# Performance work log

Measured on AMD Instinct MI355X. Metric: run time of the kernel, lower is better.

The kernel has to match this reference:

```python
import jax, jax.numpy as jnp
import numpy as np

EPS = 1e-12
W_MAX = 0.8
ALPHA_MAX = 1.5
T = 10
ETA = 0.2
ALPHA_SCALE = 1.0
N = 50000
IN_DIM = 512
HID = 256
C = 8
EH = 64
E2 = 400000  # undirected pairs; E = 2*E2 directed edges


def setup_inputs() -> dict:
    key = jax.random.key(0)
    ks = jax.random.split(key, 12)
    x = jax.random.normal(ks[0], (N, IN_DIM), jnp.float32)
    src0 = jax.random.randint(ks[1], (E2,), 0, N)
    dst0 = jax.random.randint(ks[2], (E2,), 0, N)
    edge_index = jnp.concatenate([jnp.stack([src0, dst0]), jnp.stack([dst0, src0])], axis=1)
    rev = jnp.concatenate([jnp.arange(E2) + E2, jnp.arange(E2)])
    def lin(k, i, o):
        return jax.random.normal(k, (i, o), jnp.float32) * (2.0 / i) ** 0.5
    enc_w1 = lin(ks[3], IN_DIM, HID); enc_b1 = jnp.zeros((HID,), jnp.float32)
    enc_w2 = lin(ks[4], HID, C); enc_b2 = jnp.zeros((C,), jnp.float32)
    edge_w1 = lin(ks[5], 2 * HID + 2, EH); edge_b1 = jnp.zeros((EH,), jnp.float32)
    edge_w2 = lin(ks[6], EH, 1); edge_b2 = jnp.zeros((1,), jnp.float32)
    bound = (6.0 / (C + C)) ** 0.5  # xavier_uniform
    R_raw = jax.random.uniform(ks[7], (C, C), jnp.float32, -bound, bound) + 0.5 * jnp.eye(C, dtype=jnp.float32)
    R_scale_log = jnp.float32(0.0)
    msg_logit = jnp.float32(-3.0)
    return dict(x=x, edge_index=edge_index, rev=rev,
                enc_w1=enc_w1, enc_b1=enc_b1, enc_w2=enc_w2, enc_b2=enc_b2,
                edge_w1=edge_w1, edge_b1=edge_b1, edge_w2=edge_w2, edge_b2=edge_b2,
                R_raw=R_raw, R_scale_log=R_scale_log, msg_logit=msg_logit)


def reference(x, edge_index, rev, enc_w1, enc_b1, enc_w2, enc_b2,
              edge_w1, edge_b1, edge_w2, edge_b2, R_raw, R_scale_log, msg_logit):
    num_nodes = x.shape[0]
    src, dst = edge_index[0], edge_index[1]
    # unary encoder (mlp type, eval mode -> no dropout)
    h = jax.nn.relu(x @ enc_w1 + enc_b1)
    logits = h @ enc_w2 + enc_b2
    log_phi = jax.nn.log_softmax(logits, axis=-1)  # [N, C]
    # structural edge features from out-degree of src
    deg = jax.ops.segment_sum(jnp.ones_like(src, jnp.float32), src, num_segments=num_nodes)
    logdeg = jnp.log(deg + 1.0)
    a, b = logdeg[src], logdeg[dst]
    struct = jnp.stack([a + b, jnp.abs(a - b)], axis=-1)  # [E, 2]
    # learned symmetric edge weights -> per-edge kernel K
    hs, hd = h[src], h[dst]
    edge_in = jnp.concatenate([hs * hd, jnp.abs(hs - hd), struct], axis=-1)  # [E, 2H+2]
    eh = jax.nn.relu(edge_in @ edge_w1 + edge_b1)
    w_raw = (eh @ edge_w2 + edge_b2)[:, 0]
    w = W_MAX * jax.nn.sigmoid(w_raw)
    w = 0.5 * (w + w[rev])
    R = 0.5 * (R_raw + R_raw.T)
    R = (jax.nn.softplus(R_scale_log) + 1e-06) * jnp.tanh(R)
    K = jnp.exp(w[:, None, None] * R[None])  # [E, C, C]
    degc = jnp.maximum(deg, 1.0)
    edge_norm = (degc[src] * degc[dst]) ** -0.5  # [E]
    alpha = ALPHA_MAX * jax.nn.sigmoid(msg_logit) * ALPHA_SCALE
    lp_src = log_phi[src]
    m = jax.nn.softmax(lp_src, axis=-1)  # init_unary=True

    def step(m, _):
        f = jnp.einsum('ec,ecd->ed', m, K)
        log_f = jnp.log(jnp.maximum(f, EPS)) * edge_norm[:, None]
        sum_in = jax.ops.segment_sum(log_f, dst, num_segments=num_nodes)
        excl = sum_in[src] - log_f[rev]
        m_new = jax.nn.softmax(lp_src + alpha * excl, axis=-1)
        m = (1.0 - ETA) * m + ETA * m_new
        m = jnp.maximum(m, EPS)
        m = m / m.sum(axis=-1, keepdims=True)
        return m, None

    m, _ = jax.lax.scan(step, m, None, length=T)
    # beliefs
    f = jnp.einsum('ec,ecd->ed', m, K)
    log_f = jnp.log(jnp.maximum(f, EPS)) * edge_norm[:, None]
    sum_in = jax.ops.segment_sum(log_f, dst, num_segments=num_nodes)
    beliefs = jax.nn.softmax(log_phi + alpha * sum_in, axis=-1)
    return beliefs
```

## Files before the change

### kernel.cpp

```cpp
#include <hip/hip_runtime.h>
#include <cstddef>
#include <cstdint>

typedef _Float16 h4 __attribute__((ext_vector_type(4)));
typedef _Float16 h8 __attribute__((ext_vector_type(8)));
typedef float    f4 __attribute__((ext_vector_type(4)));
typedef int      i4 __attribute__((ext_vector_type(4)));

#define NN      50000
#define IND     512
#define HIDN    256
#define E2P     400000
#define EDD     800000
#define NBLK    196
#define EBLK    1563

#define OFF_HF16    ((size_t)0)
#define OFF_LOGF    ((size_t)0)
#define OFF_Z       ((size_t)25600000)
#define OFF_DEG     ((size_t)28800000)
#define OFF_LOGDEG  ((size_t)29000000)
#define OFF_DEGC    ((size_t)29200000)
#define OFF_BASE    ((size_t)29400000)
#define OFF_CNT     ((size_t)29600000)
#define OFF_BLK     ((size_t)29800000)
#define OFF_WT      ((size_t)29804096)
#define OFF_BT      ((size_t)30066240)
#define OFF_RS      ((size_t)30135872)
#define OFF_WSYM    ((size_t)30136384)
#define OFF_POS     ((size_t)31736384)
#define OFF_ORDER   ((size_t)34936384)
#define OFF_BASE2   ((size_t)36536384)
#define OFF_OFS2    ((size_t)36736384)
#define OFF_PRC     ((size_t)36936384)
#define OFF_WN      ((size_t)43336384)
#define OFF_M       ((size_t)46536384)
#define OFF_EIS     ((size_t)59336384)
#define WS_NEED     ((size_t)62536384)

__global__ void k_deg(const int* __restrict__ ei, int* __restrict__ deg,
                      int* __restrict__ cnt2) {
    int e = blockIdx.x * 256 + threadIdx.x;
    int v = ei[e];
    atomicAdd(&deg[v], 1);
    if (e < E2P) atomicAdd(&cnt2[v], 1);
}

__global__ void k_node(const int* __restrict__ deg, float* __restrict__ logdeg,
                       float* __restrict__ degc) {
    int n = blockIdx.x * 256 + threadIdx.x;
    if (n < NN) {
        float d = (float)deg[n];
        logdeg[n] = logf(d + 1.0f);
        degc[n]   = fmaxf(d, 1.0f);
    }
}

__global__ void k_scan1(const int* __restrict__ deg, int* __restrict__ incl,
                        int* __restrict__ blk) {
    __shared__ int sm[256];
    int i = blockIdx.x * 256 + threadIdx.x;
    int v = (i < NN) ? deg[i] : 0;
    sm[threadIdx.x] = v;
    __syncthreads();
    for (int off = 1; off < 256; off <<= 1) {
        int t = (threadIdx.x >= off) ? sm[threadIdx.x - off] : 0;
        __syncthreads();
        sm[threadIdx.x] += t;
        __syncthreads();
    }
    if (i < NN) incl[i] = sm[threadIdx.x];
    if (threadIdx.x == 255) blk[blockIdx.x] = sm[255];
}

__global__ void k_scan2(int* __restrict__ blk) {
    __shared__ int sm[256];
    int v = (threadIdx.x < NBLK) ? blk[threadIdx.x] : 0;
    sm[threadIdx.x] = v;
    __syncthreads();
    for (int off = 1; off < 256; off <<= 1) {
        int t = (threadIdx.x >= off) ? sm[threadIdx.x - off] : 0;
        __syncthreads();
        sm[threadIdx.x] += t;
        __syncthreads();
    }
    if (threadIdx.x < NBLK) blk[threadIdx.x] = sm[threadIdx.x];
}

__global__ void k_scan3(const int* __restrict__ incl, const int* __restrict__ deg,
                        const int* __restrict__ blk, int* __restrict__ base) {
    int i = blockIdx.x * 256 + threadIdx.x;
    if (i < NN) {
        int off = (blockIdx.x > 0) ? blk[blockIdx.x - 1] : 0;
        base[i] = off + incl[i] - deg[i];
    }
}

__global__ void k_pos(const int* __restrict__ ei, const int* __restrict__ base,
                      int* __restrict__ cnt, int* __restrict__ pos) {
    int e = blockIdx.x * 256 + threadIdx.x;
    int dstn = ei[EDD + e];
    pos[e] = base[dstn] + atomicAdd(&cnt[dstn], 1);
}

__global__ void k_order(const int* __restrict__ ei, const int* __restrict__ base2,
                        int* __restrict__ ofs2, int* __restrict__ order) {
    int p = blockIdx.x * 256 + threadIdx.x;
    if (p < E2P) {
        int s = ei[p];
        order[base2[s] + atomicAdd(&ofs2[s], 1)] = p;
    }
}

__global__ void k_gath(const int* __restrict__ ei, const int* __restrict__ order,
                       int2* __restrict__ eiS) {
    int i = blockIdx.x * 256 + threadIdx.x;
    if (i < E2P) {
        int p = order[i];
        eiS[i] = make_int2(ei[p], ei[EDD + p]);
    }
}

__global__ void k_prep(const float* __restrict__ enc_w1, const float* __restrict__ edge_w1,
                       const float* __restrict__ R_raw, const float* __restrict__ Rsl,
                       const float* __restrict__ mlog,
                       _Float16* __restrict__ Wt, _Float16* __restrict__ Bt,
                       float* __restrict__ Rs) {
    int gid = blockIdx.x * 256 + threadIdx.x;
    if (gid < 256 * 512) {
        int n = gid >> 9, k = gid & 511;
        Wt[n * 512 + k] = (_Float16)enc_w1[k * 256 + n];
        return;
    }
    int g2 = gid - 256 * 512;
    if (g2 < 64 * 544) {
        int n = g2 / 544, k = g2 - n * 544;
        float v = 0.0f;
        if (k < 512) {
            int tm = k >> 5, r = k & 31;
            int qq = r >> 3, jj = (r >> 1) & 3, typ = k & 1;
            int c = (tm >> 1) * 32 + qq * 8 + (tm & 1) * 4 + jj;
            v = edge_w1[(typ ? 256 + c : c) * 64 + n];
        } else if (k < 514) {
            v = edge_w1[k * 64 + n];
        }
        Bt[n * 544 + k] = (_Float16)v;
        return;
    }
    int g3 = g2 - 64 * 544;
    if (g3 < 64) {
        int c = g3 >> 3, d = g3 & 7;
        float rv = 0.5f * (R_raw[c * 8 + d] + R_raw[d * 8 + c]);
        float s  = log1pf(expf(Rsl[0])) + 1e-6f;
        Rs[g3] = s * tanhf(rv);
        return;
    }
    if (g3 == 64) {
        Rs[64] = 1.5f / (1.0f + expf(-mlog[0]));
    }
}

__global__ __launch_bounds__(256) void k_enc(const float* __restrict__ x,
                                             const _Float16* __restrict__ Wt,
                                             const float* __restrict__ b1,
                                             _Float16* __restrict__ hf) {
    __shared__ _Float16 XL[64 * 40];
    __shared__ _Float16 WL[256 * 40];
    const int tid = threadIdx.x;
    const int wid = tid >> 6;
    const int lane = tid & 63;
    const int l15 = lane & 15;
    const int q = lane >> 4;
    const int m0 = blockIdx.x * 64;

    f4 acc[16];
#pragma unroll
    for (int i = 0; i < 16; i++) acc[i] = (f4){0.f, 0.f, 0.f, 0.f};

    const int xr = tid >> 2;
    const int xs = tid & 3;
    const int gr = m0 + xr;

    for (int kt = 0; kt < 16; kt++) {
        __syncthreads();
        f4 xv0 = (f4){0, 0, 0, 0}, xv1 = (f4){0, 0, 0, 0};
        if (gr < NN) {
            const f4* xp = (const f4*)(x + (size_t)gr * IND + kt * 32 + xs * 8);
            xv0 = xp[0]; xv1 = xp[1];
        }
        h8 xh;
#pragma unroll
        for (int u = 0; u < 4; u++) { xh[u] = (_Float16)xv0[u]; xh[4 + u] = (_Float16)xv1[u]; }
        *(h8*)&XL[xr * 40 + xs * 8] = xh;
#pragma unroll
        for (int rep = 0; rep < 4; rep++) {
            int cid = rep * 256 + tid;
            int n = cid >> 2;
            int off = (cid & 3) * 8;
            h8 wv = *(const h8*)(Wt + (size_t)n * IND + kt * 32 + off);
            *(h8*)&WL[n * 40 + off] = wv;
        }
        __syncthreads();
        h8 a = *(const h8*)&XL[(wid * 16 + l15) * 40 + q * 8];
#pragma unroll
        for (int nt = 0; nt < 16; nt++) {
            h8 b = *(const h8*)&WL[(nt * 16 + l15) * 40 + q * 8];
            acc[nt] = __builtin_amdgcn_mfma_f32_16x16x32_f16(a, b, acc[nt], 0, 0, 0);
        }
    }
#pragma unroll
    for (int nt = 0; nt < 16; nt++) {
        int col = nt * 16 + l15;
        float bv = b1[col];
#pragma unroll
        for (int reg = 0; reg < 4; reg++) {
            int row = m0 + wid * 16 + q * 4 + reg;
            if (row < NN) {
                float v = acc[nt][reg] + bv;
                hf[(size_t)row * HIDN + col] = (_Float16)fmaxf(v, 0.f);
            }
        }
    }
}

__global__ void k_logits(const _Float16* __restrict__ hf, const float* __restrict__ w2,
                         const float* __restrict__ b2, float* __restrict__ Z) {
    __shared__ float w2L[2048];
    for (int i = threadIdx.x; i < 2048; i += 256) w2L[i] = w2[i];
    __syncthreads();
    int n = blockIdx.x * 256 + threadIdx.x;
    if (n >= NN) return;
    float sum[8];
#pragma unroll
    for (int c = 0; c < 8; c++) sum[c] = b2[c];
    for (int kb = 0; kb < 32; kb++) {
        h8 hv = *(const h8*)(hf + (size_t)n * HIDN + kb * 8);
#pragma unroll
        for (int u = 0; u < 8; u++) {
            float hx = (float)hv[u];
            const float* wr = &w2L[(kb * 8 + u) * 8];
#pragma unroll
            for (int c = 0; c < 8; c++) sum[c] += hx * wr[c];
        }
    }
    float mx = sum[0];
#pragma unroll
    for (int c = 1; c < 8; c++) mx = fmaxf(mx, sum[c]);
    float se = 0.f;
#pragma unroll
    for (int c = 0; c < 8; c++) se += __expf(sum[c] - mx);
    float lse = __logf(se);
#pragma unroll
    for (int c = 0; c < 8; c++) Z[(size_t)n * 16 + c] = sum[c] - mx - lse;
}

__global__ __launch_bounds__(256) void k_edge(const int2* __restrict__ eiS,
        const _Float16* __restrict__ hf, const float* __restrict__ logdeg,
        const _Float16* __restrict__ BtG, const float* __restrict__ eb1,
        const float* __restrict__ ew2, const float* __restrict__ eb2,
        float* __restrict__ wsym2) {
    __shared__ _Float16 BtL[64 * 136];
    const int tid = threadIdx.x;
    const int wid = tid >> 6;
    const int lane = tid & 63;
    const int l15 = lane & 15;
    const int q = lane >> 4;
    const int eb = blockIdx.x * 128;

    int sidx[2], didx[2];
    float la[2], lb[2];
#pragma unroll
    for (int mt = 0; mt < 2; mt++) {
        int e = eb + wid * 32 + mt * 16 + l15;
        int2 sd = eiS[e];
        sidx[mt] = sd.x;
        didx[mt] = sd.y;
        la[mt] = logdeg[sidx[mt]];
        lb[mt] = logdeg[didx[mt]];
    }

    f4 acc[2][4];
#pragma unroll
    for (int a = 0; a < 2; a++)
#pragma unroll
        for (int b = 0; b < 4; b++) acc[a][b] = (f4){0.f, 0.f, 0.f, 0.f};

    const _Float16* hq = hf + q * 8;
    h8 curS[2], curD[2];
#pragma unroll
    for (int mt = 0; mt < 2; mt++) {
        curS[mt] = *(const h8*)(hq + (size_t)sidx[mt] * HIDN);
        curD[mt] = *(const h8*)(hq + (size_t)didx[mt] * HIDN);
    }

    for (int ph = 0; ph < 4; ph++) {
        __syncthreads();
        {
            const int r = tid & 63;
            const int cb = tid >> 6;
            const int kbase = ph * 128;
#pragma unroll
            for (int i = 0; i < 4; i++) {
                int ck = cb + i * 4;
                *(h8*)&BtL[r * 136 + ck * 8] =
                    *(const h8*)(BtG + (size_t)r * 544 + kbase + ck * 8);
            }
        }
        __syncthreads();
#pragma unroll
        for (int kk2 = 0; kk2 < 2; kk2++) {
            const int kk = ph * 2 + kk2;
            h8 nxtS[2], nxtD[2];
            if (kk < 7) {
                const int c1 = (kk + 1) * 32;
#pragma unroll
                for (int mt = 0; mt < 2; mt++) {
                    nxtS[mt] = *(const h8*)(hq + (size_t)sidx[mt] * HIDN + c1);
                    nxtD[mt] = *(const h8*)(hq + (size_t)didx[mt] * HIDN + c1);
                }
            }
            const int ko = kk2 * 64 + q * 8;
            {
                h8 a0[2];
#pragma unroll
                for (int mt = 0; mt < 2; mt++) {
#pragma unroll
                    for (int j = 0; j < 4; j++) {
                        float x1 = (float)curS[mt][j], x2 = (float)curD[mt][j];
                        a0[mt][2 * j]     = (_Float16)(x1 * x2);
                        a0[mt][2 * j + 1] = (_Float16)fabsf(x1 - x2);
                    }
                }
                h8 bf[4];
#pragma unroll
                for (int nt = 0; nt < 4; nt++)
                    bf[nt] = *(const h8*)&BtL[(nt * 16 + l15) * 136 + ko];
#pragma unroll
                for (int mt = 0; mt < 2; mt++)
#pragma unroll
                    for (int nt = 0; nt < 4; nt++)
                        acc[mt][nt] = __builtin_amdgcn_mfma_f32_16x16x32_f16(a0[mt], bf[nt], acc[mt][nt], 0, 0, 0);
            }
            {
                h8 a1[2];
#pragma unroll
                for (int mt = 0; mt < 2; mt++) {
#pragma unroll
                    for (int j = 0; j < 4; j++) {
                        float x1 = (float)curS[mt][4 + j], x2 = (float)curD[mt][4 + j];
                        a1[mt][2 * j]     = (_Float16)(x1 * x2);
                        a1[mt][2 * j + 1] = (_Float16)fabsf(x1 - x2);
                    }
                }
                h8 bf[4];
#pragma unroll
                for (int nt = 0; nt < 4; nt++)
                    bf[nt] = *(const h8*)&BtL[(nt * 16 + l15) * 136 + ko + 32];
#pragma unroll
                for (int mt = 0; mt < 2; mt++)
#pragma unroll
                    for (int nt = 0; nt < 4; nt++)
                        acc[mt][nt] = __builtin_amdgcn_mfma_f32_16x16x32_f16(a1[mt], bf[nt], acc[mt][nt], 0, 0, 0);
            }
            if (kk < 7) {
#pragma unroll
                for (int mt = 0; mt < 2; mt++) { curS[mt] = nxtS[mt]; curD[mt] = nxtD[mt]; }
            }
        }
    }

    __syncthreads();
    {
        const int r = tid & 63, ck = tid >> 6;
        *(h8*)&BtL[r * 136 + ck * 8] = *(const h8*)(BtG + (size_t)r * 544 + 512 + ck * 8);
    }
    __syncthreads();
    {
        h8 bf[4];
#pragma unroll
        for (int nt = 0; nt < 4; nt++)
            bf[nt] = *(const h8*)&BtL[(nt * 16 + l15) * 136 + q * 8];
#pragma unroll
        for (int mt = 0; mt < 2; mt++) {
            h8 a = (h8){0, 0, 0, 0, 0, 0, 0, 0};
            if (q == 0) {
                a[0] = (_Float16)(la[mt] + lb[mt]);
                a[1] = (_Float16)fabsf(la[mt] - lb[mt]);
            }
#pragma unroll
            for (int nt = 0; nt < 4; nt++)
                acc[mt][nt] = __builtin_amdgcn_mfma_f32_16x16x32_f16(a, bf[nt], acc[mt][nt], 0, 0, 0);
        }
    }

    float b1v[4], w2v[4];
#pragma unroll
    for (int nt = 0; nt < 4; nt++) {
        int col = nt * 16 + l15;
        b1v[nt] = eb1[col];
        w2v[nt] = ew2[col];
    }
    const float b2s = eb2[0];
    float part[2][4];
#pragma unroll
    for (int mt = 0; mt < 2; mt++)
#pragma unroll
        for (int reg = 0; reg < 4; reg++) {
            float s = 0.f;
#pragma unroll
            for (int nt = 0; nt < 4; nt++) {
                float v = acc[mt][nt][reg] + b1v[nt];
                s += fmaxf(v, 0.f) * w2v[nt];
            }
            part[mt][reg] = s;
        }
#pragma unroll
    for (int off = 1; off < 16; off <<= 1)
#pragma unroll
        for (int mt = 0; mt < 2; mt++)
#pragma unroll
            for (int reg = 0; reg < 4; reg++)
                part[mt][reg] += __shfl_xor(part[mt][reg], off, 64);
    if (l15 == 0) {
#pragma unroll
        for (int mt = 0; mt < 2; mt++)
#pragma unroll
            for (int reg = 0; reg < 4; reg++) {
                int er = eb + wid * 32 + mt * 16 + q * 4 + reg;
                if (er < E2P) {
                    float xr = part[mt][reg] + b2s;
                    wsym2[er] = 0.8f / (1.0f + __expf(-xr));
                }
            }
    }
}


__device__ __forceinline__ void kprod(const float* __restrict__ RsL, float w,
                                      const float* me, const float* mr,
                                      float* fe, float* fr) {
#pragma unroll
    for (int d = 0; d < 8; d++) { fe[d] = 0.f; fr[d] = 0.f; }
#pragma unroll
    for (int c = 0; c < 8; c++) {
        {
            float kv = __expf(w * RsL[c * 8 + c]);
            fe[c] += me[c] * kv;
            fr[c] += mr[c] * kv;
        }
#pragma unroll
        for (int d = c + 1; d < 8; d++) {
            float kv = __expf(w * RsL[c * 8 + d]);
            fe[d] += me[c] * kv; fr[d] += mr[c] * kv;
            fe[c] += me[d] * kv; fr[c] += mr[d] * kv;
        }
    }
}

__global__ __launch_bounds__(256) void k_init(const int2* __restrict__ eiS,
        const float* __restrict__ wsym2, const float* __restrict__ degc,
        const float* __restrict__ Rs, const float* __restrict__ Z,
        const int* __restrict__ pos, const int* __restrict__ order,
        i4* __restrict__ prc, float2* __restrict__ wn,
        _Float16* __restrict__ M, _Float16* __restrict__ logf) {
    __shared__ float RsL[64];
    const int tid = threadIdx.x;
    if (tid < 64) RsL[tid] = Rs[tid];
    __syncthreads();
    int i = blockIdx.x * 256 + tid;
    if (i >= E2P) return;
    int p = order[i];
    int2 sd = eiS[i];
    int sp = sd.x, dp = sd.y;
    float w = wsym2[i];
    float nrm = rsqrtf(degc[sp] * degc[dp]);
    int pz0 = pos[p], pz1 = pos[E2P + p];
    prc[i] = (i4){sp, dp, pz0, pz1};
    wn[i] = make_float2(w, nrm);
    const f4* Zs = (const f4*)(Z + (size_t)sp * 16);
    const f4* Zd = (const f4*)(Z + (size_t)dp * 16);
    f4 ls0 = Zs[0], ls1 = Zs[1], ld0 = Zd[0], ld1 = Zd[1];
    float lps[8], lpd[8];
#pragma unroll
    for (int u = 0; u < 4; u++) { lps[u] = ls0[u]; lps[4+u] = ls1[u]; lpd[u] = ld0[u]; lpd[4+u] = ld1[u]; }
    float me[8], mr[8];
    {
        float mx = lps[0], mx2 = lpd[0];
#pragma unroll
        for (int d = 1; d < 8; d++) { mx = fmaxf(mx, lps[d]); mx2 = fmaxf(mx2, lpd[d]); }
        float s = 0.f, s2 = 0.f;
#pragma unroll
        for (int d = 0; d < 8; d++) { me[d] = __expf(lps[d] - mx); s += me[d];
                                      mr[d] = __expf(lpd[d] - mx2); s2 += mr[d]; }
        float rs = 1.f / s, rs2 = 1.f / s2;
#pragma unroll
        for (int d = 0; d < 8; d++) { me[d] *= rs; mr[d] *= rs2; }
    }
    {
        h8 mh, mh2;
#pragma unroll
        for (int d = 0; d < 8; d++) { mh[d] = (_Float16)me[d]; mh2[d] = (_Float16)mr[d]; }
        *(h8*)(M + (size_t)i * 16)     = mh;
        *(h8*)(M + (size_t)i * 16 + 8) = mh2;
    }
    float fe[8], fr[8];
    kprod(RsL, w, me, mr, fe, fr);
    h8 le, lr;
#pragma unroll
    for (int d = 0; d < 8; d++) {
        le[d] = (_Float16)(__logf(fmaxf(fe[d], 1e-12f)) * nrm);
        lr[d] = (_Float16)(__logf(fmaxf(fr[d], 1e-12f)) * nrm);
    }
    *(h8*)(logf + (size_t)pz0 * 8) = le;
    *(h8*)(logf + (size_t)pz1 * 8) = lr;
}

__global__ __launch_bounds__(256) void k_bpF(const i4* __restrict__ prc,
        const float2* __restrict__ wn, const float* __restrict__ Rs,
        const float* __restrict__ Z, _Float16* __restrict__ M,
        _Float16* __restrict__ logf) {
    __shared__ float RsL[64];
    const int tid = threadIdx.x;
    if (tid < 64) RsL[tid] = Rs[tid];
    __syncthreads();
    int i = blockIdx.x * 256 + tid;
    if (i >= E2P) return;
    i4 c4 = prc[i];
    const int sp = c4[0], dp = c4[1], pz0 = c4[2], pz1 = c4[3];
    float2 wnv = wn[i];
    const float w = wnv.x, nrm = wnv.y;
    const float alpha = Rs[64];
    h8 lfh0 = *(const h8*)(logf + (size_t)pz0 * 8);
    h8 lfh1 = *(const h8*)(logf + (size_t)pz1 * 8);
    h8 mhe = *(const h8*)(M + (size_t)i * 16);
    h8 mhr = *(const h8*)(M + (size_t)i * 16 + 8);
    float me[8], mr[8], lfe[8], lfr[8];
#pragma unroll
    for (int d = 0; d < 8; d++) {
        me[d] = (float)mhe[d];  mr[d] = (float)mhr[d];
        lfe[d] = (float)lfh0[d]; lfr[d] = (float)lfh1[d];
    }
    const f4* Zs = (const f4*)(Z + (size_t)sp * 16);
    const f4* Zd = (const f4*)(Z + (size_t)dp * 16);
    f4 ls0 = Zs[0], ls1 = Zs[1], ss0 = Zs[2], ss1 = Zs[3];
    f4 ld0 = Zd[0], ld1 = Zd[1], sd0 = Zd[2], sd1 = Zd[3];
    float te[8], tr[8];
#pragma unroll
    for (int u = 0; u < 4; u++) {
        te[u]     = ls0[u] + alpha * (ss0[u] - lfr[u]);
        te[4 + u] = ls1[u] + alpha * (ss1[u] - lfr[4 + u]);
        tr[u]     = ld0[u] + alpha * (sd0[u] - lfe[u]);
        tr[4 + u] = ld1[u] + alpha * (sd1[u] - lfe[4 + u]);
    }
    float m1[8], m2[8];
    {
        float mx = te[0], mx2 = tr[0];
#pragma unroll
        for (int d = 1; d < 8; d++) { mx = fmaxf(mx, te[d]); mx2 = fmaxf(mx2, tr[d]); }
        float s = 0.f, s2 = 0.f;
#pragma unroll
        for (int d = 0; d < 8; d++) { m1[d] = __expf(te[d] - mx); s += m1[d];
                                      m2[d] = __expf(tr[d] - mx2); s2 += m2[d]; }
        float rs = 1.f / s, rs2 = 1.f / s2;
        float t1 = 0.f, t2 = 0.f;
#pragma unroll
        for (int d = 0; d < 8; d++) {
            m1[d] = fmaxf(0.8f * me[d] + 0.2f * m1[d] * rs, 1e-12f);  t1 += m1[d];
            m2[d] = fmaxf(0.8f * mr[d] + 0.2f * m2[d] * rs2, 1e-12f); t2 += m2[d];
        }
        float rt1 = 1.f / t1, rt2 = 1.f / t2;
#pragma unroll
        for (int d = 0; d < 8; d++) { m1[d] *= rt1; m2[d] *= rt2; }
    }
    {
        h8 mh, mh2;
#pragma unroll
        for (int d = 0; d < 8; d++) { mh[d] = (_Float16)m1[d]; mh2[d] = (_Float16)m2[d]; }
        *(h8*)(M + (size_t)i * 16)     = mh;
        *(h8*)(M + (size_t)i * 16 + 8) = mh2;
    }
    float fe2[8], fr2[8];
    kprod(RsL, w, m1, m2, fe2, fr2);
    h8 le, lr;
#pragma unroll
    for (int d = 0; d < 8; d++) {
        le[d] = (_Float16)(__logf(fmaxf(fe2[d], 1e-12f)) * nrm);
        lr[d] = (_Float16)(__logf(fmaxf(fr2[d], 1e-12f)) * nrm);
    }
    *(h8*)(logf + (size_t)pz0 * 8) = le;
    *(h8*)(logf + (size_t)pz1 * 8) = lr;
}

__global__ void k_sum(const _Float16* __restrict__ logf, const int* __restrict__ base,
                      const int* __restrict__ deg, float* __restrict__ Z,
                      const float* __restrict__ Rs, float* __restrict__ out, int fin) {
    int g = blockIdx.x * 256 + threadIdx.x;
    int n = g >> 3;
    if (n >= NN) return;
    int j = threadIdx.x & 7;
    int b = base[n], cnt = deg[n];
    float acc[8];
#pragma unroll
    for (int d = 0; d < 8; d++) acc[d] = 0.f;
    for (int s = j; s < cnt; s += 8) {
        h8 v = *(const h8*)(logf + (size_t)(b + s) * 8);
#pragma unroll
        for (int d = 0; d < 8; d++) acc[d] += (float)v[d];
    }
    int lane = threadIdx.x & 63;
    float v4[4], v2[2], r;
    {
        bool hi = (lane & 4) != 0;
#pragma unroll
        for (int i = 0; i < 4; i++) {
            float send = hi ? acc[i] : acc[i + 4];
            float recv = __shfl_xor(send, 4, 64);
            v4[i] = (hi ? acc[i + 4] : acc[i]) + recv;
        }
    }
    {
        bool hi = (lane & 2) != 0;
#pragma unroll
        for (int i = 0; i < 2; i++) {
            float send = hi ? v4[i] : v4[i + 2];
            float recv = __shfl_xor(send, 2, 64);
            v2[i] = (hi ? v4[i + 2] : v4[i]) + recv;
        }
    }
    {
        bool hi = (lane & 1) != 0;
        float send = hi ? v2[0] : v2[1];
        float recv = __shfl_xor(send, 1, 64);
        r = (hi ? v2[1] : v2[0]) + recv;
    }
    if (!fin) {
        Z[(size_t)n * 16 + 8 + j] = r;
    } else {
        float alpha = Rs[64];
        float v = Z[(size_t)n * 16 + j] + alpha * r;
        float mx = v;
        mx = fmaxf(mx, __shfl_xor(mx, 1, 64));
        mx = fmaxf(mx, __shfl_xor(mx, 2, 64));
        mx = fmaxf(mx, __shfl_xor(mx, 4, 64));
        float ex = __expf(v - mx);
        float s = ex;
        s += __shfl_xor(s, 1, 64); s += __shfl_xor(s, 2, 64); s += __shfl_xor(s, 4, 64);
        out[(size_t)n * 8 + j] = ex / s;
    }
}

extern "C" void kernel_launch(void* const* d_in, const int* in_sizes, int n_in,
                              void* d_out, int out_size, void* d_ws, size_t ws_size,
                              hipStream_t stream) {
    if (ws_size < WS_NEED) return;
    const float* x        = (const float*)d_in[0];
    const int*   ei       = (const int*)d_in[1];
    const float* enc_w1   = (const float*)d_in[3];
    const float* enc_b1   = (const float*)d_in[4];
    const float* enc_w2   = (const float*)d_in[5];
    const float* enc_b2   = (const float*)d_in[6];
    const float* edge_w1  = (const float*)d_in[7];
    const float* edge_b1  = (const float*)d_in[8];
    const float* edge_w2  = (const float*)d_in[9];
    const float* edge_b2  = (const float*)d_in[10];
    const float* R_raw    = (const float*)d_in[11];
    const float* Rsl      = (const float*)d_in[12];
    const float* mlog     = (const float*)d_in[13];

    char* ws = (char*)d_ws;
    _Float16* hf     = (_Float16*)(ws + OFF_HF16);
    _Float16* logfb  = (_Float16*)(ws + OFF_LOGF);
    float* Zb        = (float*)(ws + OFF_Z);
    int*   deg       = (int*)  (ws + OFF_DEG);
    float* logdeg    = (float*)(ws + OFF_LOGDEG);
    float* degc      = (float*)(ws + OFF_DEGC);
    int*   baseA     = (int*)  (ws + OFF_BASE);
    int*   cnt       = (int*)  (ws + OFF_CNT);
    int*   blk       = (int*)  (ws + OFF_BLK);
    _Float16* Wt     = (_Float16*)(ws + OFF_WT);
    _Float16* Bt     = (_Float16*)(ws + OFF_BT);
    float* Rs        = (float*)(ws + OFF_RS);
    float* wsym2     = (float*)(ws + OFF_WSYM);
    int*   pos       = (int*)  (ws + OFF_POS);
    int*   order     = (int*)  (ws + OFF_ORDER);
    int*   base2     = (int*)  (ws + OFF_BASE2);
    int*   ofs2      = (int*)  (ws + OFF_OFS2);
    i4*    prc       = (i4*)   (ws + OFF_PRC);
    float2* wnb      = (float2*)(ws + OFF_WN);
    _Float16* Mb     = (_Float16*)(ws + OFF_M);
    int2*  eiS       = (int2*) (ws + OFF_EIS);
    float* outp      = (float*)d_out;

    hipMemsetAsync(deg, 0, (size_t)NN * 4, stream);
    hipMemsetAsync(ofs2, 0, (size_t)NN * 4, stream);
    k_deg<<<dim3(EDD / 256), dim3(256), 0, stream>>>(ei, deg, ofs2);
    k_node<<<dim3(NBLK), dim3(256), 0, stream>>>(deg, logdeg, degc);
    k_prep<<<dim3((256 * 512 + 64 * 544 + 65 + 255) / 256), dim3(256), 0, stream>>>(
        enc_w1, edge_w1, R_raw, Rsl, mlog, Wt, Bt, Rs);
    k_scan1<<<dim3(NBLK), dim3(256), 0, stream>>>(deg, cnt , blk);
    k_scan2<<<dim3(1), dim3(256), 0, stream>>>(blk);
    k_scan3<<<dim3(NBLK), dim3(256), 0, stream>>>(cnt, deg, blk, baseA);
    hipMemsetAsync(cnt, 0, (size_t)NN * 4, stream);
    k_pos<<<dim3(EDD / 256), dim3(256), 0, stream>>>(ei, baseA, cnt, pos);
    k_scan1<<<dim3(NBLK), dim3(256), 0, stream>>>(ofs2, cnt, blk);
    k_scan2<<<dim3(1), dim3(256), 0, stream>>>(blk);
    k_scan3<<<dim3(NBLK), dim3(256), 0, stream>>>(cnt, ofs2, blk, base2);
    hipMemsetAsync(ofs2, 0, (size_t)NN * 4, stream);
    k_order<<<dim3(EBLK), dim3(256), 0, stream>>>(ei, base2, ofs2, order);
    k_gath<<<dim3(EBLK), dim3(256), 0, stream>>>(ei, order, eiS);
    k_enc<<<dim3((NN + 63) / 64), dim3(256), 0, stream>>>(x, Wt, enc_b1, hf);
    k_logits<<<dim3(NBLK), dim3(256), 0, stream>>>(hf, enc_w2, enc_b2, Zb);
    k_edge<<<dim3(E2P / 128), dim3(256), 0, stream>>>(eiS, hf, logdeg, Bt, edge_b1,
                                                      edge_w2, edge_b2, wsym2);
    k_init<<<dim3(EBLK), dim3(256), 0, stream>>>(eiS, wsym2, degc, Rs, Zb, pos, order,
                                                 prc, wnb, Mb, logfb);
    k_sum<<<dim3((NN * 8 + 255) / 256), dim3(256), 0, stream>>>(logfb, baseA, deg, Zb,
                                                                Rs, outp, 0);
    for (int t = 0; t < 10; t++) {
        k_bpF<<<dim3(EBLK), dim3(256), 0, stream>>>(prc, wnb, Rs, Zb, Mb, logfb);
        k_sum<<<dim3((NN * 8 + 255) / 256), dim3(256), 0, stream>>>(logfb, baseA, deg, Zb,
                                                                    Rs, outp, (t == 9) ? 1 : 0);
    }
    (void)in_sizes; (void)n_in; (void)out_size;
}
```

Before: 820.0 us.

## Sort edges by 2D src/dst bucket, recompute log_f in-step, retile encoder, swizzle XCD blocks

```diff
diff --git a/kernel.cpp b/kernel.cpp
--- a/kernel.cpp
+++ b/kernel.cpp
@@ -13,37 +13,51 @@
 #define E2P     400000
 #define EDD     800000
 #define NBLK    196
+#define SCN     50176
 #define EBLK    1563
 
 #define OFF_HF16    ((size_t)0)
 #define OFF_LOGF    ((size_t)0)
 #define OFF_Z       ((size_t)25600000)
 #define OFF_DEG     ((size_t)28800000)
-#define OFF_LOGDEG  ((size_t)29000000)
-#define OFF_DEGC    ((size_t)29200000)
-#define OFF_BASE    ((size_t)29400000)
-#define OFF_CNT     ((size_t)29600000)
-#define OFF_BLK     ((size_t)29800000)
-#define OFF_WT      ((size_t)29804096)
-#define OFF_BT      ((size_t)30066240)
-#define OFF_RS      ((size_t)30135872)
-#define OFF_WSYM    ((size_t)30136384)
-#define OFF_POS     ((size_t)31736384)
-#define OFF_ORDER   ((size_t)34936384)
-#define OFF_BASE2   ((size_t)36536384)
-#define OFF_OFS2    ((size_t)36736384)
-#define OFF_PRC     ((size_t)36936384)
-#define OFF_WN      ((size_t)43336384)
-#define OFF_M       ((size_t)46536384)
-#define OFF_EIS     ((size_t)59336384)
-#define WS_NEED     ((size_t)62536384)
+#define OFF_LOGDEG  ((size_t)29004800)
+#define OFF_DEGC    ((size_t)29204800)
+#define OFF_BASE    ((size_t)29404800)
+#define OFF_CNT     ((size_t)29609600)
+#define OFF_BLK     ((size_t)29814400)
+#define OFF_WT      ((size_t)29818496)
+#define OFF_BT      ((size_t)30080640)
+#define OFF_RS      ((size_t)30150272)
+#define OFF_WSYM    ((size_t)30150784)
+#define OFF_POS     ((size_t)31750784)
+#define OFF_ORDER   ((size_t)34950784)
+#define OFF_BASE2   ((size_t)36550784)
+#define OFF_OFS2    ((size_t)36755584)
+#define OFF_PRC     ((size_t)36960384)
+#define OFF_WN      ((size_t)43360384)
+#define OFF_M       ((size_t)46560384)
+#define OFF_EIS     ((size_t)59360384)
+#define WS_NEED     ((size_t)62560384)
+
+__device__ __forceinline__ int key2(int s, int d) {
+    return ((s >> 10) << 10) | (d >> 6);
+}
+
+__device__ __forceinline__ int xcd_swz(int bid, int nwg) {
+    int q = nwg >> 3, r = nwg & 7;
+    int x = bid & 7, idx = bid >> 3;
+    return (x < r ? x * (q + 1) : r * (q + 1) + (x - r) * q) + idx;
+}
 
 __global__ void k_deg(const int* __restrict__ ei, int* __restrict__ deg,
                       int* __restrict__ cnt2) {
     int e = blockIdx.x * 256 + threadIdx.x;
     int v = ei[e];
     atomicAdd(&deg[v], 1);
-    if (e < E2P) atomicAdd(&cnt2[v], 1);
+    if (e < E2P) {
+        int d = ei[EDD + e];
+        atomicAdd(&cnt2[key2(v, d)], 1);
+    }
 }
 
 __global__ void k_node(const int* __restrict__ deg, float* __restrict__ logdeg,
@@ -60,7 +74,7 @@
                         int* __restrict__ blk) {
     __shared__ int sm[256];
     int i = blockIdx.x * 256 + threadIdx.x;
-    int v = (i < NN) ? deg[i] : 0;
+    int v = deg[i];
     sm[threadIdx.x] = v;
     __syncthreads();
     for (int off = 1; off < 256; off <<= 1) {
@@ -69,7 +83,7 @@
         sm[threadIdx.x] += t;
         __syncthreads();
     }
-    if (i < NN) incl[i] = sm[threadIdx.x];
+    incl[i] = sm[threadIdx.x];
     if (threadIdx.x == 255) blk[blockIdx.x] = sm[255];
 }
 
@@ -90,10 +104,8 @@
 __global__ void k_scan3(const int* __restrict__ incl, const int* __restrict__ deg,
                         const int* __restrict__ blk, int* __restrict__ base) {
     int i = blockIdx.x * 256 + threadIdx.x;
-    if (i < NN) {
-        int off = (blockIdx.x > 0) ? blk[blockIdx.x - 1] : 0;
-        base[i] = off + incl[i] - deg[i];
-    }
+    int off = (blockIdx.x > 0) ? blk[blockIdx.x - 1] : 0;
+    base[i] = off + incl[i] - deg[i];
 }
 
 __global__ void k_pos(const int* __restrict__ ei, const int* __restrict__ base,
@@ -107,8 +119,8 @@
                         int* __restrict__ ofs2, int* __restrict__ order) {
     int p = blockIdx.x * 256 + threadIdx.x;
     if (p < E2P) {
-        int s = ei[p];
-        order[base2[s] + atomicAdd(&ofs2[s], 1)] = p;
+        int k = key2(ei[p], ei[EDD + p]);
+        order[base2[k] + atomicAdd(&ofs2[k], 1)] = p;
     }
 }
 
@@ -164,59 +176,84 @@
                                              const _Float16* __restrict__ Wt,
                                              const float* __restrict__ b1,
                                              _Float16* __restrict__ hf) {
-    __shared__ _Float16 XL[64 * 40];
-    __shared__ _Float16 WL[256 * 40];
+    __shared__ _Float16 XL[32 * 32];
+    __shared__ _Float16 WL[256 * 32];
     const int tid = threadIdx.x;
     const int wid = tid >> 6;
     const int lane = tid & 63;
     const int l15 = lane & 15;
     const int q = lane >> 4;
-    const int m0 = blockIdx.x * 64;
-
-    f4 acc[16];
-#pragma unroll
-    for (int i = 0; i < 16; i++) acc[i] = (f4){0.f, 0.f, 0.f, 0.f};
+    const int m0 = blockIdx.x * 32;
+    const int mt = wid & 1;
+    const int nh = wid >> 1;
+
+    f4 acc[8];
+#pragma unroll
+    for (int i = 0; i < 8; i++) acc[i] = (f4){0.f, 0.f, 0.f, 0.f};
 
     const int xr = tid >> 2;
     const int xs = tid & 3;
+    const bool xact = (tid < 128);
     const int gr = m0 + xr;
+
+    h8 xreg = (h8){0, 0, 0, 0, 0, 0, 0, 0};
+    if (xact && gr < NN) {
+        const f4* xp = (const f4*)(x + (size_t)gr * IND + xs * 8);
+        f4 a0 = xp[0], a1 = xp[1];
+#pragma unroll
+        for (int u = 0; u < 4; u++) { xreg[u] = (_Float16)a0[u]; xreg[4 + u] = (_Float16)a1[u]; }
+    }
+    h8 wreg[4];
+#pragma unroll
+    for (int rep = 0; rep < 4; rep++) {
+        int id = rep * 256 + tid;
+        int n = id >> 2, c = id & 3;
+        wreg[rep] = *(const h8*)(Wt + (size_t)n * IND + c * 8);
+    }
 
     for (int kt = 0; kt < 16; kt++) {
         __syncthreads();
-        f4 xv0 = (f4){0, 0, 0, 0}, xv1 = (f4){0, 0, 0, 0};
-        if (gr < NN) {
-            const f4* xp = (const f4*)(x + (size_t)gr * IND + kt * 32 + xs * 8);
-            xv0 = xp[0]; xv1 = xp[1];
-        }
-        h8 xh;
-#pragma unroll
-        for (int u = 0; u < 4; u++) { xh[u] = (_Float16)xv0[u]; xh[4 + u] = (_Float16)xv1[u]; }
-        *(h8*)&XL[xr * 40 + xs * 8] = xh;
+        if (xact) *(h8*)&XL[xr * 32 + ((xs + (xr >> 1)) & 3) * 8] = xreg;
 #pragma unroll
         for (int rep = 0; rep < 4; rep++) {
-            int cid = rep * 256 + tid;
-            int n = cid >> 2;
-            int off = (cid & 3) * 8;
-            h8 wv = *(const h8*)(Wt + (size_t)n * IND + kt * 32 + off);
-            *(h8*)&WL[n * 40 + off] = wv;
+            int id = rep * 256 + tid;
+            int n = id >> 2, c = id & 3;
+            *(h8*)&WL[n * 32 + ((c + (n >> 1)) & 3) * 8] = wreg[rep];
         }
         __syncthreads();
-        h8 a = *(const h8*)&XL[(wid * 16 + l15) * 40 + q * 8];
-#pragma unroll
-        for (int nt = 0; nt < 16; nt++) {
-            h8 b = *(const h8*)&WL[(nt * 16 + l15) * 40 + q * 8];
-            acc[nt] = __builtin_amdgcn_mfma_f32_16x16x32_f16(a, b, acc[nt], 0, 0, 0);
-        }
-    }
-#pragma unroll
-    for (int nt = 0; nt < 16; nt++) {
-        int col = nt * 16 + l15;
+        if (kt < 15) {
+            const int kc = (kt + 1) * 32;
+            if (xact && gr < NN) {
+                const f4* xp = (const f4*)(x + (size_t)gr * IND + kc + xs * 8);
+                f4 a0 = xp[0], a1 = xp[1];
+#pragma unroll
+                for (int u = 0; u < 4; u++) { xreg[u] = (_Float16)a0[u]; xreg[4 + u] = (_Float16)a1[u]; }
+            }
+#pragma unroll
+            for (int rep = 0; rep < 4; rep++) {
+                int id = rep * 256 + tid;
+                int n = id >> 2, c = id & 3;
+                wreg[rep] = *(const h8*)(Wt + (size_t)n * IND + kc + c * 8);
+            }
+        }
+        const int ar = mt * 16 + l15;
+        h8 a = *(const h8*)&XL[ar * 32 + ((q + (ar >> 1)) & 3) * 8];
+#pragma unroll
+        for (int nt8 = 0; nt8 < 8; nt8++) {
+            int r2 = (nh * 8 + nt8) * 16 + l15;
+            h8 b = *(const h8*)&WL[r2 * 32 + ((q + (r2 >> 1)) & 3) * 8];
+            acc[nt8] = __builtin_amdgcn_mfma_f32_16x16x32_f16(a, b, acc[nt8], 0, 0, 0);
+        }
+    }
+#pragma unroll
+    for (int nt8 = 0; nt8 < 8; nt8++) {
+        int col = (nh * 8 + nt8) * 16 + l15;
         float bv = b1[col];
 #pragma unroll
         for (int reg = 0; reg < 4; reg++) {
-            int row = m0 + wid * 16 + q * 4 + reg;
+            int row = m0 + mt * 16 + q * 4 + reg;
             if (row < NN) {
-                float v = acc[nt][reg] + bv;
+                float v = acc[nt8][reg] + bv;
                 hf[(size_t)row * HIDN + col] = (_Float16)fmaxf(v, 0.f);
             }
         }
@@ -265,7 +302,7 @@
     const int lane = tid & 63;
     const int l15 = lane & 15;
     const int q = lane >> 4;
-    const int eb = blockIdx.x * 128;
+    const int eb = xcd_swz(blockIdx.x, gridDim.x) * 128;
 
     int sidx[2], didx[2];
     float la[2], lb[2];
@@ -296,12 +333,12 @@
     for (int ph = 0; ph < 4; ph++) {
         __syncthreads();
         {
-            const int r = tid & 63;
-            const int cb = tid >> 6;
+            const int r = tid >> 2;
+            const int c0 = tid & 3;
             const int kbase = ph * 128;
 #pragma unroll
-            for (int i = 0; i < 4; i++) {
-                int ck = cb + i * 4;
+            for (int i2 = 0; i2 < 4; i2++) {
+                int ck = c0 + i2 * 4;
                 *(h8*)&BtL[r * 136 + ck * 8] =
                     *(const h8*)(BtG + (size_t)r * 544 + kbase + ck * 8);
             }
@@ -371,7 +408,7 @@
 
     __syncthreads();
     {
-        const int r = tid & 63, ck = tid >> 6;
+        const int r = tid >> 2, ck = tid & 3;
         *(h8*)&BtL[r * 136 + ck * 8] = *(const h8*)(BtG + (size_t)r * 544 + 512 + ck * 8);
     }
     __syncthreads();
@@ -467,7 +504,7 @@
     const int tid = threadIdx.x;
     if (tid < 64) RsL[tid] = Rs[tid];
     __syncthreads();
-    int i = blockIdx.x * 256 + tid;
+    int i = xcd_swz(blockIdx.x, EBLK) * 256 + tid;
     if (i >= E2P) return;
     int p = order[i];
     int2 sd = eiS[i];
@@ -523,22 +560,25 @@
     const int tid = threadIdx.x;
     if (tid < 64) RsL[tid] = Rs[tid];
     __syncthreads();
-    int i = blockIdx.x * 256 + tid;
+    int i = xcd_swz(blockIdx.x, EBLK) * 256 + tid;
     if (i >= E2P) return;
     i4 c4 = prc[i];
     const int sp = c4[0], dp = c4[1], pz0 = c4[2], pz1 = c4[3];
     float2 wnv = wn[i];
     const float w = wnv.x, nrm = wnv.y;
     const float alpha = Rs[64];
-    h8 lfh0 = *(const h8*)(logf + (size_t)pz0 * 8);
-    h8 lfh1 = *(const h8*)(logf + (size_t)pz1 * 8);
     h8 mhe = *(const h8*)(M + (size_t)i * 16);
     h8 mhr = *(const h8*)(M + (size_t)i * 16 + 8);
-    float me[8], mr[8], lfe[8], lfr[8];
+    float me[8], mr[8];
+#pragma unroll
+    for (int d = 0; d < 8; d++) { me[d] = (float)mhe[d]; mr[d] = (float)mhr[d]; }
+    float fe[8], fr[8];
+    kprod(RsL, w, me, mr, fe, fr);
+    float lfe[8], lfr[8];
 #pragma unroll
     for (int d = 0; d < 8; d++) {
-        me[d] = (float)mhe[d];  mr[d] = (float)mhr[d];
-        lfe[d] = (float)lfh0[d]; lfr[d] = (float)lfh1[d];
+        lfe[d] = __logf(fmaxf(fe[d], 1e-12f)) * nrm;
+        lfr[d] = __logf(fmaxf(fr[d], 1e-12f)) * nrm;
     }
     const f4* Zs = (const f4*)(Z + (size_t)sp * 16);
     const f4* Zd = (const f4*)(Z + (size_t)dp * 16);
@@ -691,8 +731,8 @@
     int2*  eiS       = (int2*) (ws + OFF_EIS);
     float* outp      = (float*)d_out;
 
-    hipMemsetAsync(deg, 0, (size_t)NN * 4, stream);
-    hipMemsetAsync(ofs2, 0, (size_t)NN * 4, stream);
+    hipMemsetAsync(deg, 0, (size_t)SCN * 4, stream);
+    hipMemsetAsync(ofs2, 0, (size_t)SCN * 4, stream);
     k_deg<<<dim3(EDD / 256), dim3(256), 0, stream>>>(ei, deg, ofs2);
     k_node<<<dim3(NBLK), dim3(256), 0, stream>>>(deg, logdeg, degc);
     k_prep<<<dim3((256 * 512 + 64 * 544 + 65 + 255) / 256), dim3(256), 0, stream>>>(
@@ -700,15 +740,15 @@
     k_scan1<<<dim3(NBLK), dim3(256), 0, stream>>>(deg, cnt , blk);
     k_scan2<<<dim3(1), dim3(256), 0, stream>>>(blk);
     k_scan3<<<dim3(NBLK), dim3(256), 0, stream>>>(cnt, deg, blk, baseA);
-    hipMemsetAsync(cnt, 0, (size_t)NN * 4, stream);
+    hipMemsetAsync(cnt, 0, (size_t)SCN * 4, stream);
     k_pos<<<dim3(EDD / 256), dim3(256), 0, stream>>>(ei, baseA, cnt, pos);
     k_scan1<<<dim3(NBLK), dim3(256), 0, stream>>>(ofs2, cnt, blk);
     k_scan2<<<dim3(1), dim3(256), 0, stream>>>(blk);
     k_scan3<<<dim3(NBLK), dim3(256), 0, stream>>>(cnt, ofs2, blk, base2);
-    hipMemsetAsync(ofs2, 0, (size_t)NN * 4, stream);
+    hipMemsetAsync(ofs2, 0, (size_t)SCN * 4, stream);
     k_order<<<dim3(EBLK), dim3(256), 0, stream>>>(ei, base2, ofs2, order);
     k_gath<<<dim3(EBLK), dim3(256), 0, stream>>>(ei, order, eiS);
-    k_enc<<<dim3((NN + 63) / 64), dim3(256), 0, stream>>>(x, Wt, enc_b1, hf);
+    k_enc<<<dim3((NN + 31) / 32), dim3(256), 0, stream>>>(x, Wt, enc_b1, hf);
     k_logits<<<dim3(NBLK), dim3(256), 0, stream>>>(hf, enc_w2, enc_b2, Zb);
     k_edge<<<dim3(E2P / 128), dim3(256), 0, stream>>>(eiS, hf, logdeg, Bt, edge_b1,
                                                       edge_w2, edge_b2, wsym2);
```

Result: no change. 806.4 us (-1.7%).
